# Optimization experiments

Hardware: AMD Instinct MI355X
Metric: run time of the kernel (lower is better)

## Reference

```python
import jax, jax.numpy as jnp
import numpy as np
from functools import partial

SEQ, BATCH, IN, HID = 512, 128, 256, 1024


def setup_inputs() -> dict:
    key = jax.random.key(0)
    ks = jax.random.split(key, 8)
    std = 1.0 / np.sqrt(HID)
    u = lambda k, shape: jax.random.uniform(k, shape, jnp.float32, -std, std)
    return {
        "inp": jax.random.normal(ks[0], (SEQ, BATCH, IN), jnp.float32),
        "Wxh": u(ks[1], (4 * HID, IN)),
        "bxh": u(ks[2], (4 * HID,)),
        "Whh": u(ks[3], (4 * HID, HID)),
        "bhh": u(ks[4], (4 * HID,)),
        "Wout": u(ks[5], (IN, HID)),
        "bout": u(ks[6], (IN,)),
    }


def lstm_forward(inp, Wxh, bxh, Whh, bhh, Wout, bout):
    seq, batch, _ = inp.shape
    hid = Whh.shape[1]
    # Precompute input projection for all timesteps: [T, B, 4H]
    x_proj = jnp.einsum("tbi,gi->tbg", inp, Wxh) + bxh

    def step(carry, xp_t):
        h, c = carry
        gates = xp_t + h @ Whh.T + bhh            # [B, 4H]
        i, f, g, o = jnp.split(gates, 4, axis=-1)  # torch chunk order: i,f,g,o
        c = jax.nn.sigmoid(f) * c + jax.nn.sigmoid(i) * jnp.tanh(g)
        h = jax.nn.sigmoid(o) * jnp.tanh(c)
        return (h, c), h

    h0 = jnp.zeros((batch, hid), inp.dtype)
    c0 = jnp.zeros((batch, hid), inp.dtype)
    _, hs = jax.lax.scan(step, (h0, c0), x_proj)   # hs: [T, B, H]
    out = jnp.einsum("tbh,ih->tbi", hs, Wout) + bout
    return jax.nn.log_softmax(out, axis=-1)


def reference(inp, Wxh, bxh, Whh, bhh, Wout, bout):
    return lstm_forward(inp, Wxh, bxh, Whh, bhh, Wout, bout)
```

## Files before the change

kernel.cpp:

```cpp
#include <hip/hip_runtime.h>
#include <math.h>


#define TT  512
#define BB  128
#define NIN 256
#define NH  1024
#define G4  4096
#define KK  1280

typedef __bf16 bf16_t;
typedef bf16_t bf16x8 __attribute__((ext_vector_type(8)));
typedef float  f32x4  __attribute__((ext_vector_type(4)));

#define MFMA(a, b, c) __builtin_amdgcn_mfma_f32_16x16x32_bf16((a), (b), (c), 0, 0, 0)


__global__ void conv_w_kernel(const float* __restrict__ Wxh,
                              const float* __restrict__ Whh,
                              bf16_t* __restrict__ Wc) {
  const int n = blockIdx.y;
  const int k = blockIdx.x * 256 + threadIdx.x;
  const int g = n & 3, j = n >> 2;
  float v = (k < NIN) ? Wxh[(size_t)(g * NH + j) * NIN + k]
                      : Whh[(size_t)(g * NH + j) * NH + (k - NIN)];
  Wc[(size_t)n * KK + k] = (bf16_t)v;
}

__global__ void conv_f2b_kernel(const float* __restrict__ src,
                                bf16_t* __restrict__ dst, int n4) {
  int i = blockIdx.x * 256 + threadIdx.x;
  if (i < n4) {
    float4 v = ((const float4*)src)[i];
    dst[i * 4 + 0] = (bf16_t)v.x;
    dst[i * 4 + 1] = (bf16_t)v.y;
    dst[i * 4 + 2] = (bf16_t)v.z;
    dst[i * 4 + 3] = (bf16_t)v.w;
  }
}

__global__ void prep_bias_kernel(const float* __restrict__ bxh,
                                 const float* __restrict__ bhh,
                                 float* __restrict__ bsum4) {
  int n = blockIdx.x * 256 + threadIdx.x;
  int g = n & 3, j = n >> 2;
  bsum4[n] = bxh[g * NH + j] + bhh[g * NH + j];
}


__global__ __launch_bounds__(256) void fused_step(
    int t,
    const bf16_t* __restrict__ x_bf,
    const bf16_t* __restrict__ Wc,
    const float*  __restrict__ bsum4,
    const bf16_t* __restrict__ h_cur,
    bf16_t*       __restrict__ h_next,
    float*        __restrict__ c,
    const bf16_t* __restrict__ WoutB,
    const float*  __restrict__ bout,
    float*        __restrict__ logits_w,
    const float*  __restrict__ logits_r,
    float*        __restrict__ out)
{
  const int blk  = blockIdx.x;
  const int tid  = threadIdx.x;
  const int lane = tid & 63;
  const int wv   = tid >> 6;
  const int l16  = lane & 15;
  const int lq   = lane >> 4;

  if (blk < 128) {
    if (t >= TT) return;
    __shared__ float gs[64 * 68];

    const int mb    = (blk & 1) * 64;
    const int ns    = blk >> 1;
    const int nbase = ns * 64;
    const int wm = wv & 1, wn = wv >> 1;
    const int m0 = mb + wm * 32;
    const int n0 = nbase + wn * 32;

    const bf16_t* ax  = x_bf + (size_t)t * BB * NIN + (size_t)(m0 + l16) * NIN + lq * 8;
    const bf16_t* ah  = h_cur + (size_t)(m0 + l16) * NH + lq * 8;
    const bf16_t* b0p = Wc + (size_t)(n0 + l16) * KK + lq * 8;
    const bf16_t* b1p = Wc + (size_t)(n0 + 16 + l16) * KK + lq * 8;

    f32x4 a00 = {0,0,0,0}, a01 = {0,0,0,0}, a10 = {0,0,0,0}, a11 = {0,0,0,0};

#pragma unroll
    for (int kk = 0; kk < 8; ++kk) {
      bf16x8 r0 = *(const bf16x8*)(ax + kk * 32);
      bf16x8 r1 = *(const bf16x8*)(ax + 16 * NIN + kk * 32);
      bf16x8 b0 = *(const bf16x8*)(b0p + kk * 32);
      bf16x8 b1 = *(const bf16x8*)(b1p + kk * 32);
      a00 = MFMA(r0, b0, a00); a01 = MFMA(r0, b1, a01);
      a10 = MFMA(r1, b0, a10); a11 = MFMA(r1, b1, a11);
    }
#pragma unroll 8
    for (int kk = 0; kk < 32; ++kk) {
      bf16x8 r0 = *(const bf16x8*)(ah + kk * 32);
      bf16x8 r1 = *(const bf16x8*)(ah + 16 * NH + kk * 32);
      bf16x8 b0 = *(const bf16x8*)(b0p + NIN + kk * 32);
      bf16x8 b1 = *(const bf16x8*)(b1p + NIN + kk * 32);
      a00 = MFMA(r0, b0, a00); a01 = MFMA(r0, b1, a01);
      a10 = MFMA(r1, b0, a10); a11 = MFMA(r1, b1, a11);
    }

#pragma unroll
    for (int r = 0; r < 4; ++r) {
      const int rr0 = wm * 32 + lq * 4 + r;
      gs[rr0 * 68 + wn * 32 + l16]             = a00[r];
      gs[rr0 * 68 + wn * 32 + 16 + l16]        = a01[r];
      gs[(rr0 + 16) * 68 + wn * 32 + l16]      = a10[r];
      gs[(rr0 + 16) * 68 + wn * 32 + 16 + l16] = a11[r];
    }
    __syncthreads();

    const int b_l = tid >> 2;
#pragma unroll
    for (int p = 0; p < 4; ++p) {
      const int jl = (tid & 3) + p * 4;
      const int j  = ns * 16 + jl;
      float4 g4 = *(const float4*)&gs[b_l * 68 + jl * 4];
      float4 bs = ((const float4*)bsum4)[j];
      const float gi = g4.x + bs.x;
      const float gf = g4.y + bs.y;
      const float gg = g4.z + bs.z;
      const float go = g4.w + bs.w;
      const float si = 1.f / (1.f + __expf(-gi));
      const float sf = 1.f / (1.f + __expf(-gf));
      const float so = 1.f / (1.f + __expf(-go));
      const size_t idx = (size_t)(mb + b_l) * NH + j;
      const float cn = sf * c[idx] + si * tanhf(gg);
      c[idx] = cn;
      h_next[idx] = (bf16_t)(so * tanhf(cn));
    }
  } else if (blk < 160) {
    if (t < 1 || t > TT) return;
    const int gw  = (blk - 128) * 4 + wv;
    const int bm0 = (gw >> 4) * 16;
    const int bn0 = (gw & 15) * 16;

    const bf16_t* ap = h_cur + (size_t)(bm0 + l16) * NH + lq * 8;
    const bf16_t* bp = WoutB + (size_t)(bn0 + l16) * NH + lq * 8;
    f32x4 acc = {0,0,0,0};
#pragma unroll 8
    for (int kk = 0; kk < 32; ++kk) {
      bf16x8 a = *(const bf16x8*)(ap + kk * 32);
      bf16x8 b = *(const bf16x8*)(bp + kk * 32);
      acc = MFMA(a, b, acc);
    }
    const float bo = bout[bn0 + l16];
#pragma unroll
    for (int r = 0; r < 4; ++r)
      logits_w[(size_t)(bm0 + lq * 4 + r) * NIN + bn0 + l16] = acc[r] + bo;
  } else {
    if (t < 2) return;
    __shared__ float red[2][4][4];
    const int b0 = (blk - 160) * 4;
    float v[4], mx[4], sm[4];
#pragma unroll
    for (int r = 0; r < 4; ++r) v[r] = logits_r[(size_t)(b0 + r) * NIN + tid];
#pragma unroll
    for (int r = 0; r < 4; ++r) mx[r] = v[r];
#pragma unroll
    for (int off = 32; off > 0; off >>= 1)
#pragma unroll
      for (int r = 0; r < 4; ++r) mx[r] = fmaxf(mx[r], __shfl_xor(mx[r], off));
    if (lane == 0)
#pragma unroll
      for (int r = 0; r < 4; ++r) red[0][wv][r] = mx[r];
    __syncthreads();
#pragma unroll
    for (int r = 0; r < 4; ++r)
      mx[r] = fmaxf(fmaxf(red[0][0][r], red[0][1][r]),
                    fmaxf(red[0][2][r], red[0][3][r]));
#pragma unroll
    for (int r = 0; r < 4; ++r) sm[r] = __expf(v[r] - mx[r]);
#pragma unroll
    for (int off = 32; off > 0; off >>= 1)
#pragma unroll
      for (int r = 0; r < 4; ++r) sm[r] += __shfl_xor(sm[r], off);
    if (lane == 0)
#pragma unroll
      for (int r = 0; r < 4; ++r) red[1][wv][r] = sm[r];
    __syncthreads();
    float* ot = out + (size_t)(t - 2) * BB * NIN + (size_t)b0 * NIN;
#pragma unroll
    for (int r = 0; r < 4; ++r) {
      float S = red[1][0][r] + red[1][1][r] + red[1][2][r] + red[1][3][r];
      ot[(size_t)r * NIN + tid] = v[r] - mx[r] - logf(S);
    }
  }
}


extern "C" void kernel_launch(void* const* d_in, const int* in_sizes, int n_in,
                              void* d_out, int out_size, void* d_ws, size_t ws_size,
                              hipStream_t stream) {
  const float* inp  = (const float*)d_in[0];
  const float* Wxh  = (const float*)d_in[1];
  const float* bxh  = (const float*)d_in[2];
  const float* Whh  = (const float*)d_in[3];
  const float* bhh  = (const float*)d_in[4];
  const float* Wout = (const float*)d_in[5];
  const float* bout = (const float*)d_in[6];
  float* out = (float*)d_out;

  char* p = (char*)d_ws;
  bf16_t* Wc    = (bf16_t*)p; p += (size_t)G4 * KK * 2;
  bf16_t* x_bf  = (bf16_t*)p; p += (size_t)TT * BB * NIN * 2;
  bf16_t* WoutB = (bf16_t*)p; p += (size_t)NIN * NH * 2;
  bf16_t* h0    = (bf16_t*)p; p += (size_t)BB * NH * 2;
  bf16_t* h1    = (bf16_t*)p; p += (size_t)BB * NH * 2;
  float*  cbuf  = (float*)p;  p += (size_t)BB * NH * 4;
  float*  bsum4 = (float*)p;  p += (size_t)G4 * 4;
  float*  lg0   = (float*)p;  p += (size_t)BB * NIN * 4;
  float*  lg1   = (float*)p;  p += (size_t)BB * NIN * 4;

  conv_w_kernel<<<dim3(KK / 256, G4), 256, 0, stream>>>(Wxh, Whh, Wc);
  conv_f2b_kernel<<<(TT * BB * NIN / 4 + 255) / 256, 256, 0, stream>>>(
      inp, x_bf, TT * BB * NIN / 4);
  conv_f2b_kernel<<<(NIN * NH / 4 + 255) / 256, 256, 0, stream>>>(
      Wout, WoutB, NIN * NH / 4);
  prep_bias_kernel<<<G4 / 256, 256, 0, stream>>>(bxh, bhh, bsum4);
  hipMemsetAsync(h0, 0, (size_t)BB * NH * 2, stream);
  hipMemsetAsync(cbuf, 0, (size_t)BB * NH * 4, stream);

  bf16_t* hb[2] = {h0, h1};
  float*  lg[2] = {lg0, lg1};
  for (int t = 0; t < TT + 2; ++t) {
    fused_step<<<192, 256, 0, stream>>>(
        t, x_bf, Wc, bsum4,
        hb[t & 1], hb[(t + 1) & 1], cbuf,
        WoutB, bout,
        lg[t & 1],
        lg[(t + 1) & 1],
        out);
  }
}
```

Before: 11.14 ms.

## Split recurrent GEMM K dimension across two wave groups with 512-thread blocks

Doubles the block size to 512 threads. In the gate blocks, the second group of four waves takes part of the hidden-state K range, and the two partial results are summed through two shared-memory buffers. Each K-half gets 20 of the 40 32-wide K chunks (8 input plus 12 hidden versus 20 hidden), which shortens the serial MFMA chain per wave on the latency-bound recurrent step. Grid size drops from 192 to 160 because the output-projection and softmax blocks each now do double work. Costs are a larger shared-memory footprint, an extra LDS read and add per gate, and more threads per block.

```diff
diff --git a/kernel.cpp b/kernel.cpp
--- a/kernel.cpp
+++ b/kernel.cpp
@@ -48,7 +48,7 @@
 }
 
 
-__global__ __launch_bounds__(256) void fused_step(
+__global__ __launch_bounds__(512) void fused_step(
     int t,
     const bf16_t* __restrict__ x_bf,
     const bf16_t* __restrict__ Wc,
@@ -71,12 +71,12 @@
 
   if (blk < 128) {
     if (t >= TT) return;
-    __shared__ float gs[64 * 68];
+    __shared__ float gs[2][64 * 68];
 
     const int mb    = (blk & 1) * 64;
     const int ns    = blk >> 1;
     const int nbase = ns * 64;
-    const int wm = wv & 1, wn = wv >> 1;
+    const int wm = wv & 1, wn = (wv >> 1) & 1, kh = wv >> 2;
     const int m0 = mb + wm * 32;
     const int n0 = nbase + wn * 32;
 
@@ -87,46 +87,60 @@
 
     f32x4 a00 = {0,0,0,0}, a01 = {0,0,0,0}, a10 = {0,0,0,0}, a11 = {0,0,0,0};
 
-#pragma unroll
-    for (int kk = 0; kk < 8; ++kk) {
-      bf16x8 r0 = *(const bf16x8*)(ax + kk * 32);
-      bf16x8 r1 = *(const bf16x8*)(ax + 16 * NIN + kk * 32);
-      bf16x8 b0 = *(const bf16x8*)(b0p + kk * 32);
-      bf16x8 b1 = *(const bf16x8*)(b1p + kk * 32);
-      a00 = MFMA(r0, b0, a00); a01 = MFMA(r0, b1, a01);
-      a10 = MFMA(r1, b0, a10); a11 = MFMA(r1, b1, a11);
-    }
-#pragma unroll 8
-    for (int kk = 0; kk < 32; ++kk) {
-      bf16x8 r0 = *(const bf16x8*)(ah + kk * 32);
-      bf16x8 r1 = *(const bf16x8*)(ah + 16 * NH + kk * 32);
-      bf16x8 b0 = *(const bf16x8*)(b0p + NIN + kk * 32);
-      bf16x8 b1 = *(const bf16x8*)(b1p + NIN + kk * 32);
-      a00 = MFMA(r0, b0, a00); a01 = MFMA(r0, b1, a01);
-      a10 = MFMA(r1, b0, a10); a11 = MFMA(r1, b1, a11);
-    }
-
+    if (kh == 0) {
+#pragma unroll
+      for (int kk = 0; kk < 8; ++kk) {
+        bf16x8 r0 = *(const bf16x8*)(ax + kk * 32);
+        bf16x8 r1 = *(const bf16x8*)(ax + 16 * NIN + kk * 32);
+        bf16x8 b0 = *(const bf16x8*)(b0p + kk * 32);
+        bf16x8 b1 = *(const bf16x8*)(b1p + kk * 32);
+        a00 = MFMA(r0, b0, a00); a01 = MFMA(r0, b1, a01);
+        a10 = MFMA(r1, b0, a10); a11 = MFMA(r1, b1, a11);
+      }
+#pragma unroll 6
+      for (int kk = 0; kk < 12; ++kk) {
+        bf16x8 r0 = *(const bf16x8*)(ah + kk * 32);
+        bf16x8 r1 = *(const bf16x8*)(ah + 16 * NH + kk * 32);
+        bf16x8 b0 = *(const bf16x8*)(b0p + NIN + kk * 32);
+        bf16x8 b1 = *(const bf16x8*)(b1p + NIN + kk * 32);
+        a00 = MFMA(r0, b0, a00); a01 = MFMA(r0, b1, a01);
+        a10 = MFMA(r1, b0, a10); a11 = MFMA(r1, b1, a11);
+      }
+    } else {
+#pragma unroll 5
+      for (int kk = 12; kk < 32; ++kk) {
+        bf16x8 r0 = *(const bf16x8*)(ah + kk * 32);
+        bf16x8 r1 = *(const bf16x8*)(ah + 16 * NH + kk * 32);
+        bf16x8 b0 = *(const bf16x8*)(b0p + NIN + kk * 32);
+        bf16x8 b1 = *(const bf16x8*)(b1p + NIN + kk * 32);
+        a00 = MFMA(r0, b0, a00); a01 = MFMA(r0, b1, a01);
+        a10 = MFMA(r1, b0, a10); a11 = MFMA(r1, b1, a11);
+      }
+    }
+
+    float* g = gs[kh];
 #pragma unroll
     for (int r = 0; r < 4; ++r) {
       const int rr0 = wm * 32 + lq * 4 + r;
-      gs[rr0 * 68 + wn * 32 + l16]             = a00[r];
-      gs[rr0 * 68 + wn * 32 + 16 + l16]        = a01[r];
-      gs[(rr0 + 16) * 68 + wn * 32 + l16]      = a10[r];
-      gs[(rr0 + 16) * 68 + wn * 32 + 16 + l16] = a11[r];
+      g[rr0 * 68 + wn * 32 + l16]             = a00[r];
+      g[rr0 * 68 + wn * 32 + 16 + l16]        = a01[r];
+      g[(rr0 + 16) * 68 + wn * 32 + l16]      = a10[r];
+      g[(rr0 + 16) * 68 + wn * 32 + 16 + l16] = a11[r];
     }
     __syncthreads();
 
-    const int b_l = tid >> 2;
-#pragma unroll
-    for (int p = 0; p < 4; ++p) {
-      const int jl = (tid & 3) + p * 4;
+    const int b_l = tid >> 3;
+#pragma unroll
+    for (int p = 0; p < 2; ++p) {
+      const int jl = (tid & 7) + p * 8;
       const int j  = ns * 16 + jl;
-      float4 g4 = *(const float4*)&gs[b_l * 68 + jl * 4];
+      float4 g0 = *(const float4*)&gs[0][b_l * 68 + jl * 4];
+      float4 g1 = *(const float4*)&gs[1][b_l * 68 + jl * 4];
       float4 bs = ((const float4*)bsum4)[j];
-      const float gi = g4.x + bs.x;
-      const float gf = g4.y + bs.y;
-      const float gg = g4.z + bs.z;
-      const float go = g4.w + bs.w;
+      const float gi = g0.x + g1.x + bs.x;
+      const float gf = g0.y + g1.y + bs.y;
+      const float gg = g0.z + g1.z + bs.z;
+      const float go = g0.w + g1.w + bs.w;
       const float si = 1.f / (1.f + __expf(-gi));
       const float sf = 1.f / (1.f + __expf(-gf));
       const float so = 1.f / (1.f + __expf(-go));
@@ -135,9 +149,9 @@
       c[idx] = cn;
       h_next[idx] = (bf16_t)(so * tanhf(cn));
     }
-  } else if (blk < 160) {
+  } else if (blk < 144) {
     if (t < 1 || t > TT) return;
-    const int gw  = (blk - 128) * 4 + wv;
+    const int gw  = (blk - 128) * 8 + wv;
     const int bm0 = (gw >> 4) * 16;
     const int bn0 = (gw & 15) * 16;
 
@@ -156,11 +170,14 @@
       logits_w[(size_t)(bm0 + lq * 4 + r) * NIN + bn0 + l16] = acc[r] + bo;
   } else {
     if (t < 2) return;
-    __shared__ float red[2][4][4];
-    const int b0 = (blk - 160) * 4;
+    __shared__ float red[2][2][4][4];
+    const int sub  = tid >> 8;
+    const int stid = tid & 255;
+    const int swv  = (tid >> 6) & 3;
+    const int b0 = (blk - 144) * 8 + sub * 4;
     float v[4], mx[4], sm[4];
 #pragma unroll
-    for (int r = 0; r < 4; ++r) v[r] = logits_r[(size_t)(b0 + r) * NIN + tid];
+    for (int r = 0; r < 4; ++r) v[r] = logits_r[(size_t)(b0 + r) * NIN + stid];
 #pragma unroll
     for (int r = 0; r < 4; ++r) mx[r] = v[r];
 #pragma unroll
@@ -169,12 +186,12 @@
       for (int r = 0; r < 4; ++r) mx[r] = fmaxf(mx[r], __shfl_xor(mx[r], off));
     if (lane == 0)
 #pragma unroll
-      for (int r = 0; r < 4; ++r) red[0][wv][r] = mx[r];
+      for (int r = 0; r < 4; ++r) red[0][sub][swv][r] = mx[r];
     __syncthreads();
 #pragma unroll
     for (int r = 0; r < 4; ++r)
-      mx[r] = fmaxf(fmaxf(red[0][0][r], red[0][1][r]),
-                    fmaxf(red[0][2][r], red[0][3][r]));
+      mx[r] = fmaxf(fmaxf(red[0][sub][0][r], red[0][sub][1][r]),
+                    fmaxf(red[0][sub][2][r], red[0][sub][3][r]));
 #pragma unroll
     for (int r = 0; r < 4; ++r) sm[r] = __expf(v[r] - mx[r]);
 #pragma unroll
@@ -183,13 +200,14 @@
       for (int r = 0; r < 4; ++r) sm[r] += __shfl_xor(sm[r], off);
     if (lane == 0)
 #pragma unroll
-      for (int r = 0; r < 4; ++r) red[1][wv][r] = sm[r];
+      for (int r = 0; r < 4; ++r) red[1][sub][swv][r] = sm[r];
     __syncthreads();
     float* ot = out + (size_t)(t - 2) * BB * NIN + (size_t)b0 * NIN;
 #pragma unroll
     for (int r = 0; r < 4; ++r) {
-      float S = red[1][0][r] + red[1][1][r] + red[1][2][r] + red[1][3][r];
-      ot[(size_t)r * NIN + tid] = v[r] - mx[r] - logf(S);
+      float S = red[1][sub][0][r] + red[1][sub][1][r] +
+                red[1][sub][2][r] + red[1][sub][3][r];
+      ot[(size_t)r * NIN + stid] = v[r] - mx[r] - logf(S);
     }
   }
 }
@@ -230,7 +248,7 @@
   bf16_t* hb[2] = {h0, h1};
   float*  lg[2] = {lg0, lg1};
   for (int t = 0; t < TT + 2; ++t) {
-    fused_step<<<192, 256, 0, stream>>>(
+    fused_step<<<160, 512, 0, stream>>>(
         t, x_bf, Wc, bsum4,
         hb[t & 1], hb[(t + 1) & 1], cbuf,
         WoutB, bout,
```

Result: faster. 10.82 ms (-2.8%).
